# Kernel optimization log

Hardware: AMD Instinct MI355X
Metric: run time of the kernel (lower is better)

## Reference

```python
import jax, jax.numpy as jnp
import numpy as np

CUTOFF = 6.0   # matches init cutoff
D = 32         # descriptor/MLP width
NTYPES = 3     # len(type_map)


def setup_inputs() -> dict:
    key = jax.random.key(0)
    ks = jax.random.split(key, 13)
    b, n, m, n_ghost = 2, 8192, 64, 512
    neighbor_vectors = jax.random.normal(ks[0], (b, n, m, 4), jnp.float32)
    element_map = jax.random.randint(ks[1], (b, n), 0, NTYPES, jnp.int32)
    central_atoms = jax.random.randint(ks[2], (b, n), 0, n, jnp.int32)
    neighbor_indices = jax.random.randint(ks[3], (b, n, m), 0, n + n_ghost, jnp.int32)
    neighbor_types = jax.random.randint(ks[4], (b, n, m), 0, NTYPES, jnp.int32)
    type_embed = 0.1 * jax.random.normal(ks[5], (NTYPES, D), jnp.float32)
    elem_bias = 0.1 * jax.random.normal(ks[6], (NTYPES,), jnp.float32)
    W1 = 0.5 * jax.random.normal(ks[7], (4, D), jnp.float32)
    b1 = 0.1 * jax.random.normal(ks[8], (D,), jnp.float32)
    W2 = (1.0 / np.sqrt(D)) * jax.random.normal(ks[9], (D, D), jnp.float32)
    b2 = 0.1 * jax.random.normal(ks[10], (D,), jnp.float32)
    W3 = (1.0 / np.sqrt(D)) * jax.random.normal(ks[11], (D, 1), jnp.float32)
    b3 = 0.1 * jax.random.normal(ks[12], (1,), jnp.float32)
    return dict(element_map=element_map, central_atoms=central_atoms,
                neighbor_indices=neighbor_indices, neighbor_types=neighbor_types,
                neighbor_vectors=neighbor_vectors, n_ghost=n_ghost,
                type_embed=type_embed, elem_bias=elem_bias,
                W1=W1, b1=b1, W2=W2, b2=b2, W3=W3, b3=b3)


def _field_Ei(rel, element_map, neighbor_types, type_embed, elem_bias, W1, b1, W2, b2, W3, b3):
    # rel: [b,n,m,3] relative positions; recompute distance as the torch forward does
    dist = jnp.linalg.norm(rel, axis=-1, keepdims=True)                 # [b,n,m,1]
    fc = 0.5 * (jnp.cos(jnp.pi * jnp.minimum(dist, CUTOFF) / CUTOFF) + 1.0)
    s = jnp.exp(-dist) * fc                                             # smooth radial weight
    feat = jnp.concatenate([s, s * rel], axis=-1)                       # [b,n,m,4]
    h = jnp.tanh(feat @ W1 + b1 + type_embed[neighbor_types])           # [b,n,m,D]
    g = h.mean(axis=2)                                                  # pool over neighbors -> [b,n,D]
    h2 = jnp.tanh(g @ W2 + b2)                                          # [b,n,D]
    Ei = h2 @ W3 + b3 + elem_bias[element_map][..., None]               # [b,n,1]
    return Ei


def derive_mechanics(grad_Ei, neighbor_vectors, neighbor_indices, n_ghost):
    # grad_Ei: [b,n,m,3] = d(sum Ei)/d r_ij, with r_ij = r_j - r_i
    b, n, m, _ = grad_Ei.shape
    ntot = n + n_ghost
    bidx = jnp.arange(b)[:, None, None]
    # force on central atom i: +sum_j dE/dr_ij ; reaction scattered to neighbor j: -dE/dr_ij
    force = jnp.zeros((b, ntot, 3), grad_Ei.dtype)
    force = force.at[:, :n].add(grad_Ei.sum(axis=2))
    force = force.at[bidx, neighbor_indices].add(-grad_Ei)
    rij = neighbor_vectors[..., 1:]                                     # [b,n,m,3]
    pv = (rij[..., :, None] * grad_Ei[..., None, :]).reshape(b, n, m, 9)  # pair virial r (x) dE
    virial = pv.sum(axis=(1, 2))                                        # [b,9]
    av = jnp.zeros((b, ntot, 9), grad_Ei.dtype)
    av = av.at[bidx, neighbor_indices].add(pv)
    return force[:, :n], virial, av[:, :n]


def reference(element_map, central_atoms, neighbor_indices, neighbor_types,
              neighbor_vectors, n_ghost, type_embed, elem_bias,
              W1, b1, W2, b2, W3, b3):
    rel = neighbor_vectors[..., 1:]                                     # [b,n,m,3]

    def ei_sum(r):
        Ei = _field_Ei(r, element_map, neighbor_types, type_embed, elem_bias,
                       W1, b1, W2, b2, W3, b3)
        return Ei.sum(), Ei

    grad_Ei, Ei = jax.grad(ei_sum, has_aux=True)(rel)                   # matches autograd.grad w/ ones mask
    Etot = Ei.sum(axis=1)                                               # [b,1]
    dist = jnp.linalg.norm(rel, axis=-1, keepdims=True)
    nv = jnp.concatenate([dist, rel], axis=-1)
    force, virial, atomic_virial = derive_mechanics(grad_Ei, nv, neighbor_indices, n_ghost)
    return Etot, Ei, force, virial, atomic_virial
```

## Files before the change

### kernel.cpp

```cpp
#include <hip/hip_runtime.h>

#define CUTOFF_F 6.0f
#define PI_F 3.14159265358979323846f
#define CAP 112
#define EXCAP 8192

typedef __fp16 fp16x2 __attribute__((ext_vector_type(2)));

__device__ __forceinline__ unsigned pk2(float a, float b) {
  union { fp16x2 h; unsigned u; } cv;
  cv.h = __builtin_amdgcn_cvt_pkrtz(a, b);
  return cv.u;
}
__device__ __forceinline__ float f16bits(unsigned v) {
  union { unsigned short u; __fp16 h; } cv; cv.u = (unsigned short)v; return (float)cv.h;
}

template<int CTRL>
__device__ __forceinline__ float dpp_add(float x) {
  int y = __builtin_amdgcn_update_dpp(0, __float_as_int(x), CTRL, 0xf, 0xf, true);
  return x + __int_as_float(y);
}
__device__ __forceinline__ float wave_sum63(float x) {
  x = dpp_add<0x111>(x);
  x = dpp_add<0x112>(x);
  x = dpp_add<0x114>(x);
  x = dpp_add<0x118>(x);
  x = dpp_add<0x142>(x);
  x = dpp_add<0x143>(x);
  return x;
}

__device__ __forceinline__ float fast_tanh(float x) {
  float e = __expf(2.0f * x);
  return 1.0f - 2.0f * __builtin_amdgcn_rcpf(e + 1.0f);
}

__global__ __launch_bounds__(256) void field_zero(
    int* __restrict__ counts, int* __restrict__ ecount, int bn) {
  const int i = blockIdx.x * 256 + threadIdx.x;
  if (i < bn) counts[i] = 0;
  if (i == 0) ecount[0] = 0;
}

__global__ __launch_bounds__(256) void field_main(
    const int* __restrict__ element_map,
    const int* __restrict__ neighbor_indices,
    const int* __restrict__ neighbor_types,
    const float4* __restrict__ neighbor_vectors,
    const float* __restrict__ type_embed,
    const float* __restrict__ elem_bias,
    const float* __restrict__ W1,
    const float* __restrict__ b1,
    const float* __restrict__ W2,
    const float* __restrict__ b2,
    const float* __restrict__ W3,
    const float* __restrict__ b3,
    float* __restrict__ outEi,
    int* __restrict__ counts,
    int* __restrict__ ecount,
    float4* __restrict__ extras,
    float4* __restrict__ bucket,
    float* __restrict__ partials,
    int n)
{
  __shared__ float4 sW1t[32];
  __shared__ float  sbte[3][32];
  __shared__ float  sW2[32 * 33];
  __shared__ float  sW3[32];
  __shared__ float  sb2[32];
  __shared__ float  sElemBias[3];
  __shared__ float  sb3;
  __shared__ float  blkEi[4];
  __shared__ float  blkVir[4][9];
  __shared__ unsigned hb[4][64][9];
  __shared__ float    gtd[4][3][32];

  const int tid = threadIdx.x;

  if (tid < 32) {
    sW1t[tid] = make_float4(W1[tid], W1[32 + tid], W1[64 + tid], W1[96 + tid]);
    sW3[tid]  = W3[tid];
    sb2[tid]  = b2[tid];
  } else if (tid < 128) {
    int t = (tid - 32) >> 5, k = tid & 31;
    sbte[t][k] = b1[k] + type_embed[t * 32 + k];
  } else if (tid == 128) {
    sb3 = b3[0];
  } else if (tid < 132) {
    sElemBias[tid - 129] = elem_bias[tid - 129];
  }
  for (int i = tid; i < 1024; i += 256) {
    int l = i >> 5, k = i & 31;
    sW2[l * 33 + k] = W2[i];
  }
  __syncthreads();

  const int wave = tid >> 6;
  const int lane = tid & 63;
  const int atom = blockIdx.x * 4 + wave;
  const int bb = atom / n;

  const int base = atom * 64 + lane;
  const int idx = neighbor_indices[base];
  const int dest = bb * n + idx;
  const int em = element_map[atom];

  int pos = 0;
  const bool real = (idx < n);
  if (real) pos = atomicAdd(&counts[dest], 1);

  const float4 nv = neighbor_vectors[base];
  const float rx = nv.y, ry = nv.z, rz = nv.w;
  const int typ = neighbor_types[base];

  const float d2 = rx * rx + ry * ry + rz * rz;
  const float d = sqrtf(d2);
  const float invd = (d > 0.0f) ? __builtin_amdgcn_rcpf(d) : 0.0f;
  float s, sp;
  if (d < CUTOFF_F) {
    const float arg = d * (PI_F / CUTOFF_F);
    const float cs = __cosf(arg);
    const float sn = __sinf(arg);
    const float e = __expf(-d);
    const float fc = 0.5f * (cs + 1.0f);
    const float fcp = -(0.5f * PI_F / CUTOFF_F) * sn;
    s = e * fc;
    sp = e * (fcp - fc);
  } else {
    s = 0.0f;
    sp = 0.0f;
  }
  const float f1 = s * rx, f2 = s * ry, f3 = s * rz;

  float h[32];
  const int dim = lane & 15;
  const int q   = lane >> 4;
  const int w   = dim >> 1;
  const int sh  = (dim & 1) << 4;

#pragma unroll
  for (int pass = 0; pass < 2; ++pass) {
    const int kb = pass << 4;
#pragma unroll
    for (int k = 0; k < 16; k += 2) {
      const float4 wa = sW1t[kb + k];
      float pa = sbte[typ][kb + k];
      pa = fmaf(s, wa.x, pa); pa = fmaf(f1, wa.y, pa);
      pa = fmaf(f2, wa.z, pa); pa = fmaf(f3, wa.w, pa);
      h[kb + k] = fast_tanh(pa);
      const float4 wb = sW1t[kb + k + 1];
      float pb = sbte[typ][kb + k + 1];
      pb = fmaf(s, wb.x, pb); pb = fmaf(f1, wb.y, pb);
      pb = fmaf(f2, wb.z, pb); pb = fmaf(f3, wb.w, pb);
      h[kb + k + 1] = fast_tanh(pb);
      hb[wave][lane][k >> 1] = pk2(h[kb + k], h[kb + k + 1]);
    }
    float s0 = 0.0f, s1 = 0.0f;
#pragma unroll
    for (int jj = 0; jj < 16; jj += 2) {
      s0 += f16bits(hb[wave][(q << 4) + jj][w] >> sh);
      s1 += f16bits(hb[wave][(q << 4) + jj + 1][w] >> sh);
    }
    float gs = s0 + s1;
    gs += __shfl_xor(gs, 16);
    gs += __shfl_xor(gs, 32);
    if (lane < 16) gtd[wave][0][kb + lane] = gs * (1.0f / 64.0f);
  }

  const int kd = lane & 31;
  float a0 = sb2[kd], a1 = 0.0f, a2 = 0.0f, a3 = 0.0f;
#pragma unroll
  for (int l = 0; l < 8; l += 4) {
    const float4 gA = *(const float4*)&gtd[wave][0][l];
    const float4 gB = *(const float4*)&gtd[wave][0][l + 8];
    const float4 gC = *(const float4*)&gtd[wave][0][l + 16];
    const float4 gD = *(const float4*)&gtd[wave][0][l + 24];
    a0 = fmaf(gA.x, sW2[(l + 0) * 33 + kd], a0);
    a0 = fmaf(gA.y, sW2[(l + 1) * 33 + kd], a0);
    a0 = fmaf(gA.z, sW2[(l + 2) * 33 + kd], a0);
    a0 = fmaf(gA.w, sW2[(l + 3) * 33 + kd], a0);
    a1 = fmaf(gB.x, sW2[(l + 8) * 33 + kd], a1);
    a1 = fmaf(gB.y, sW2[(l + 9) * 33 + kd], a1);
    a1 = fmaf(gB.z, sW2[(l + 10) * 33 + kd], a1);
    a1 = fmaf(gB.w, sW2[(l + 11) * 33 + kd], a1);
    a2 = fmaf(gC.x, sW2[(l + 16) * 33 + kd], a2);
    a2 = fmaf(gC.y, sW2[(l + 17) * 33 + kd], a2);
    a2 = fmaf(gC.z, sW2[(l + 18) * 33 + kd], a2);
    a2 = fmaf(gC.w, sW2[(l + 19) * 33 + kd], a2);
    a3 = fmaf(gD.x, sW2[(l + 24) * 33 + kd], a3);
    a3 = fmaf(gD.y, sW2[(l + 25) * 33 + kd], a3);
    a3 = fmaf(gD.z, sW2[(l + 26) * 33 + kd], a3);
    a3 = fmaf(gD.w, sW2[(l + 27) * 33 + kd], a3);
  }
  const float acc = (a0 + a1) + (a2 + a3);
  const float h2 = fast_tanh(acc);
  const float tl = (1.0f - h2 * h2) * sW3[kd];
  if (lane < 32) gtd[wave][1][kd] = tl;

  float b0 = 0.0f, b1v = 0.0f, b2v = 0.0f, b3v = 0.0f;
#pragma unroll
  for (int l = 0; l < 8; l += 4) {
    const float4 tA = *(const float4*)&gtd[wave][1][l];
    const float4 tB = *(const float4*)&gtd[wave][1][l + 8];
    const float4 tC = *(const float4*)&gtd[wave][1][l + 16];
    const float4 tD = *(const float4*)&gtd[wave][1][l + 24];
    b0 = fmaf(tA.x, sW2[kd * 33 + l + 0], b0);
    b0 = fmaf(tA.y, sW2[kd * 33 + l + 1], b0);
    b0 = fmaf(tA.z, sW2[kd * 33 + l + 2], b0);
    b0 = fmaf(tA.w, sW2[kd * 33 + l + 3], b0);
    b1v = fmaf(tB.x, sW2[kd * 33 + l + 8], b1v);
    b1v = fmaf(tB.y, sW2[kd * 33 + l + 9], b1v);
    b1v = fmaf(tB.z, sW2[kd * 33 + l + 10], b1v);
    b1v = fmaf(tB.w, sW2[kd * 33 + l + 11], b1v);
    b2v = fmaf(tC.x, sW2[kd * 33 + l + 16], b2v);
    b2v = fmaf(tC.y, sW2[kd * 33 + l + 17], b2v);
    b2v = fmaf(tC.z, sW2[kd * 33 + l + 18], b2v);
    b2v = fmaf(tC.w, sW2[kd * 33 + l + 19], b2v);
    b3v = fmaf(tD.x, sW2[kd * 33 + l + 24], b3v);
    b3v = fmaf(tD.y, sW2[kd * 33 + l + 25], b3v);
    b3v = fmaf(tD.z, sW2[kd * 33 + l + 26], b3v);
    b3v = fmaf(tD.w, sW2[kd * 33 + l + 27], b3v);
  }
  if (lane < 32) gtd[wave][2][kd] = ((b0 + b1v) + (b2v + b3v)) * (1.0f / 64.0f);

  float p = h2 * sW3[kd];

  float q0 = 0.0f, q1 = 0.0f, q2 = 0.0f, q3 = 0.0f;
#pragma unroll
  for (int k = 0; k < 32; k += 4) {
    const float4 d4 = *(const float4*)&gtd[wave][2][k];
#pragma unroll
    for (int u = 0; u < 4; ++u) {
      const float dgk = (u == 0) ? d4.x : (u == 1) ? d4.y : (u == 2) ? d4.z : d4.w;
      const float hk = h[k + u];
      const float dpre = dgk * (1.0f - hk * hk);
      const float4 wv = sW1t[k + u];
      q0 = fmaf(dpre, wv.x, q0);
      q1 = fmaf(dpre, wv.y, q1);
      q2 = fmaf(dpre, wv.z, q2);
      q3 = fmaf(dpre, wv.w, q3);
    }
  }

  const float common = sp * invd * (q0 + q1 * rx + q2 * ry + q3 * rz);
  const float gx = fmaf(common, rx, s * q1);
  const float gy = fmaf(common, ry, s * q2);
  const float gz = fmaf(common, rz, s * q3);

  if (real) {
    float4 pay;
    pay.x = __uint_as_float(pk2(gx, gy));
    pay.y = __uint_as_float(pk2(gz, rx));
    pay.z = __uint_as_float(pk2(ry, rz));
    if (pos < CAP) {
      pay.w = 0.0f;
      bucket[(size_t)dest * CAP + pos] = pay;
    } else {
      const int ep = atomicAdd(ecount, 1);
      if (ep < EXCAP) {
        pay.w = __int_as_float(dest);
        extras[ep] = pay;
      }
    }
  }

  float sfx = wave_sum63(gx);
  float sfy = wave_sum63(gy);
  float sfz = wave_sum63(gz);
  float vr0 = wave_sum63(rx * gx), vr1 = wave_sum63(rx * gy), vr2 = wave_sum63(rx * gz);
  float vr3 = wave_sum63(ry * gx), vr4 = wave_sum63(ry * gy), vr5 = wave_sum63(ry * gz);
  float vr6 = wave_sum63(rz * gx), vr7 = wave_sum63(rz * gy), vr8 = wave_sum63(rz * gz);
  float psum = wave_sum63(p) * 0.5f;

  if (lane == 63) {
    const float Ei_val = psum + sb3 + sElemBias[em];
    outEi[atom] = Ei_val;
    blkEi[wave] = Ei_val;
    blkVir[wave][0] = vr0; blkVir[wave][1] = vr1; blkVir[wave][2] = vr2;
    blkVir[wave][3] = vr3; blkVir[wave][4] = vr4; blkVir[wave][5] = vr5;
    blkVir[wave][6] = vr6; blkVir[wave][7] = vr7; blkVir[wave][8] = vr8;
    float4 pay;
    pay.x = __uint_as_float(pk2(-sfx, -sfy));
    pay.y = __uint_as_float(pk2(-sfz, 0.0f));
    pay.z = 0.0f;
    const int spos = atomicAdd(&counts[atom], 1);
    if (spos < CAP) {
      pay.w = 0.0f;
      bucket[(size_t)atom * CAP + spos] = pay;
    } else {
      const int ep = atomicAdd(ecount, 1);
      if (ep < EXCAP) {
        pay.w = __int_as_float(atom);
        extras[ep] = pay;
      }
    }
  }

  __syncthreads();
  if (tid < 9) {
    partials[blockIdx.x * 10 + tid] =
        blkVir[0][tid] + blkVir[1][tid] + blkVir[2][tid] + blkVir[3][tid];
  } else if (tid == 9) {
    partials[blockIdx.x * 10 + 9] = blkEi[0] + blkEi[1] + blkEi[2] + blkEi[3];
  }
}

__global__ __launch_bounds__(256) void field_gather(
    const int* __restrict__ counts,
    const int* __restrict__ ecount,
    const float4* __restrict__ extras,
    const float4* __restrict__ bucket,
    const float* __restrict__ partials,
    float* __restrict__ outForce,
    float* __restrict__ outAV,
    float* __restrict__ outEtot,
    float* __restrict__ outVirial,
    int half)
{
  __shared__ float sf[4][12];
  __shared__ float sacc[4][10];
  const int tid = threadIdx.x;
  const int wave = tid >> 6;
  const int lane = tid & 63;
  const int dest = blockIdx.x * 4 + wave;

  const int rawcnt = counts[dest];
  const int cnt = (rawcnt > CAP) ? CAP : rawcnt;
  const int ec0 = *ecount;

  float fx = 0.0f, fy = 0.0f, fz = 0.0f;
  float a0 = 0, a1 = 0, a2 = 0, a3 = 0, a4 = 0, a5 = 0, a6 = 0, a7 = 0, a8 = 0;

#pragma unroll 2
  for (int l = lane; l < cnt; l += 64) {
    const float4 pay = bucket[(size_t)dest * CAP + l];
    const unsigned w0 = __float_as_uint(pay.x);
    const unsigned w1 = __float_as_uint(pay.y);
    const unsigned w2 = __float_as_uint(pay.z);
    const float gx = f16bits(w0), gy = f16bits(w0 >> 16);
    const float gz = f16bits(w1), rx = f16bits(w1 >> 16);
    const float ry = f16bits(w2), rz = f16bits(w2 >> 16);
    fx -= gx; fy -= gy; fz -= gz;
    a0 = fmaf(rx, gx, a0); a1 = fmaf(rx, gy, a1); a2 = fmaf(rx, gz, a2);
    a3 = fmaf(ry, gx, a3); a4 = fmaf(ry, gy, a4); a5 = fmaf(ry, gz, a5);
    a6 = fmaf(rz, gx, a6); a7 = fmaf(rz, gy, a7); a8 = fmaf(rz, gz, a8);
  }

  if (ec0 > 0) {
    const int ec = (ec0 < EXCAP) ? ec0 : EXCAP;
    for (int t = lane; t < ec; t += 64) {
      const float4 ex = extras[t];
      if (__float_as_int(ex.w) == dest) {
        const unsigned w0 = __float_as_uint(ex.x);
        const unsigned w1 = __float_as_uint(ex.y);
        const unsigned w2 = __float_as_uint(ex.z);
        const float gx = f16bits(w0), gy = f16bits(w0 >> 16);
        const float gz = f16bits(w1), rx = f16bits(w1 >> 16);
        const float ry = f16bits(w2), rz = f16bits(w2 >> 16);
        fx -= gx; fy -= gy; fz -= gz;
        a0 = fmaf(rx, gx, a0); a1 = fmaf(rx, gy, a1); a2 = fmaf(rx, gz, a2);
        a3 = fmaf(ry, gx, a3); a4 = fmaf(ry, gy, a4); a5 = fmaf(ry, gz, a5);
        a6 = fmaf(rz, gx, a6); a7 = fmaf(rz, gy, a7); a8 = fmaf(rz, gz, a8);
      }
    }
  }

  fx = wave_sum63(fx); fy = wave_sum63(fy); fz = wave_sum63(fz);
  a0 = wave_sum63(a0); a1 = wave_sum63(a1); a2 = wave_sum63(a2);
  a3 = wave_sum63(a3); a4 = wave_sum63(a4); a5 = wave_sum63(a5);
  a6 = wave_sum63(a6); a7 = wave_sum63(a7); a8 = wave_sum63(a8);

  if (lane == 63) {
    sf[wave][0] = fx; sf[wave][1] = fy; sf[wave][2] = fz;
    sf[wave][3] = a0; sf[wave][4] = a1; sf[wave][5] = a2;
    sf[wave][6] = a3; sf[wave][7] = a4; sf[wave][8] = a5;
    sf[wave][9] = a6; sf[wave][10] = a7; sf[wave][11] = a8;
  }
  __syncthreads();

  const int d0 = blockIdx.x * 4;
  if (tid < 12) {
    outForce[(size_t)d0 * 3 + tid] = sf[tid / 3][tid % 3];
  } else if (tid >= 64 && tid < 100) {
    const int t = tid - 64;
    outAV[(size_t)d0 * 9 + t] = sf[t / 9][3 + t % 9];
  }

  if (blockIdx.x < 2) {
    const int b = blockIdx.x;
    float acc[10] = {0, 0, 0, 0, 0, 0, 0, 0, 0, 0};
    for (int r = b * half + tid; r < (b + 1) * half; r += 256) {
#pragma unroll
      for (int t = 0; t < 10; ++t) acc[t] += partials[r * 10 + t];
    }
#pragma unroll
    for (int t = 0; t < 10; ++t) acc[t] = wave_sum63(acc[t]);
    if (lane == 63) {
#pragma unroll
      for (int t = 0; t < 10; ++t) sacc[wave][t] = acc[t];
    }
    __syncthreads();
    if (tid < 9) {
      outVirial[b * 9 + tid] = sacc[0][tid] + sacc[1][tid] + sacc[2][tid] + sacc[3][tid];
    } else if (tid == 9) {
      outEtot[b] = sacc[0][9] + sacc[1][9] + sacc[2][9] + sacc[3][9];
    }
  }
}

extern "C" void kernel_launch(void* const* d_in, const int* in_sizes, int n_in,
                              void* d_out, int out_size, void* d_ws, size_t ws_size,
                              hipStream_t stream) {
  const int* element_map        = (const int*)d_in[0];
  const int* neighbor_indices   = (const int*)d_in[2];
  const int* neighbor_types     = (const int*)d_in[3];
  const float4* neighbor_vectors = (const float4*)d_in[4];
  const float* type_embed = (const float*)d_in[6];
  const float* elem_bias  = (const float*)d_in[7];
  const float* W1 = (const float*)d_in[8];
  const float* b1 = (const float*)d_in[9];
  const float* W2 = (const float*)d_in[10];
  const float* b2 = (const float*)d_in[11];
  const float* W3 = (const float*)d_in[12];
  const float* b3 = (const float*)d_in[13];

  const int B = 2;
  const int bn = in_sizes[0];
  const int n = bn / B;
  const int nblk = bn / 4;

  float* out = (float*)d_out;
  float* outEtot   = out;
  float* outEi     = outEtot + B;
  float* outForce  = outEi + bn;
  float* outVirial = outForce + (size_t)bn * 3;
  float* outAV     = outVirial + (size_t)B * 9;

  char* ws = (char*)d_ws;
  int* counts = (int*)ws;
  size_t countBytes = (size_t)bn * sizeof(int);
  int* ecount = (int*)(ws + countBytes);
  size_t ecountBytes = 16;
  float4* extras = (float4*)(ws + countBytes + ecountBytes);
  size_t extrasBytes = (size_t)EXCAP * sizeof(float4);
  float* partials = (float*)(ws + countBytes + ecountBytes + extrasBytes);
  size_t partialBytes = (size_t)nblk * 10 * sizeof(float);
  float4* bucket = (float4*)(ws + countBytes + ecountBytes + extrasBytes + partialBytes);

  dim3 block(256);
  hipLaunchKernelGGL(field_zero, dim3((bn + 255) / 256), block, 0, stream,
                     counts, ecount, bn);
  hipLaunchKernelGGL(field_main, dim3(nblk), block, 0, stream,
                     element_map, neighbor_indices, neighbor_types,
                     neighbor_vectors, type_embed, elem_bias,
                     W1, b1, W2, b2, W3, b3,
                     outEi, counts, ecount, extras, bucket, partials, n);
  hipLaunchKernelGGL(field_gather, dim3(nblk), block, 0, stream,
                     counts, ecount, extras, bucket, partials,
                     outForce, outAV, outEtot, outVirial, nblk / B);
}
```

Before: 147.6 us.

## Use packed fp16 dot2 and half2 math for per-neighbor MLP forward/backward

After: 148.9 us. No clear change (+0.8%).

```diff
diff --git a/kernel.cpp b/kernel.cpp
--- a/kernel.cpp
+++ b/kernel.cpp
@@ -5,15 +5,28 @@
 #define CAP 112
 #define EXCAP 8192
 
-typedef __fp16 fp16x2 __attribute__((ext_vector_type(2)));
+typedef __fp16   fp16x2 __attribute__((ext_vector_type(2)));
+typedef _Float16 h2f    __attribute__((ext_vector_type(2)));
+
+union hcv { unsigned u; fp16x2 b; h2f a; };
+__device__ __forceinline__ unsigned as_u(h2f x)   { hcv c; c.a = x; return c.u; }
+__device__ __forceinline__ h2f      u2a(unsigned v){ hcv c; c.u = v; return c.a; }
+__device__ __forceinline__ fp16x2   u2b(unsigned v){ hcv c; c.u = v; return c.b; }
 
 __device__ __forceinline__ unsigned pk2(float a, float b) {
-  union { fp16x2 h; unsigned u; } cv;
-  cv.h = __builtin_amdgcn_cvt_pkrtz(a, b);
-  return cv.u;
+  hcv c; c.b = __builtin_amdgcn_cvt_pkrtz(a, b); return c.u;
 }
 __device__ __forceinline__ float f16bits(unsigned v) {
   union { unsigned short u; __fp16 h; } cv; cv.u = (unsigned short)v; return (float)cv.h;
+}
+
+__device__ __forceinline__ float FDOT2(unsigned a, unsigned b, float c) {
+#if defined(__has_builtin) && __has_builtin(__builtin_amdgcn_fdot2)
+  return __builtin_amdgcn_fdot2(u2b(a), u2b(b), c, false);
+#else
+  h2f x = u2a(a), y = u2a(b);
+  return fmaf((float)x.x, (float)y.x, fmaf((float)x.y, (float)y.y, c));
+#endif
 }
 
 template<int CTRL>
@@ -64,35 +77,51 @@
     float* __restrict__ partials,
     int n)
 {
-  __shared__ float4 sW1t[32];
-  __shared__ float  sbte[3][32];
-  __shared__ float  sW2[32 * 33];
+  __shared__ uint4  sW1f[16];
+  __shared__ uint4  sW1b[16];
+  __shared__ unsigned sW2h[16*33];
+  __shared__ unsigned sW2d[32*17];
+  __shared__ float2 sbte2[3][16];
   __shared__ float  sW3[32];
   __shared__ float  sb2[32];
   __shared__ float  sElemBias[3];
   __shared__ float  sb3;
   __shared__ float  blkEi[4];
   __shared__ float  blkVir[4][9];
-  __shared__ unsigned hb[4][64][9];
-  __shared__ float    gtd[4][3][32];
+  __shared__ unsigned hb[4][64][5];
+  __shared__ unsigned sgp[4][16];
+  __shared__ unsigned stl[4][16];
+  __shared__ unsigned sdg[4][16];
 
   const int tid = threadIdx.x;
 
-  if (tid < 32) {
-    sW1t[tid] = make_float4(W1[tid], W1[32 + tid], W1[64 + tid], W1[96 + tid]);
-    sW3[tid]  = W3[tid];
-    sb2[tid]  = b2[tid];
-  } else if (tid < 128) {
-    int t = (tid - 32) >> 5, k = tid & 31;
-    sbte[t][k] = b1[k] + type_embed[t * 32 + k];
-  } else if (tid == 128) {
+  if (tid < 32) { sW3[tid] = W3[tid]; sb2[tid] = b2[tid]; }
+  if (tid < 16) {
+    const int k0 = 2*tid, k1 = 2*tid + 1;
+    sW1f[tid] = make_uint4(pk2(W1[k0],    W1[32+k0]),
+                           pk2(W1[64+k0], W1[96+k0]),
+                           pk2(W1[k1],    W1[32+k1]),
+                           pk2(W1[64+k1], W1[96+k1]));
+  } else if (tid < 32) {
+    const int p = tid - 16, k0 = 2*p, k1 = 2*p + 1;
+    sW1b[p] = make_uint4(pk2(W1[k0],    W1[k1]),
+                         pk2(W1[32+k0], W1[32+k1]),
+                         pk2(W1[64+k0], W1[64+k1]),
+                         pk2(W1[96+k0], W1[96+k1]));
+  } else if (tid < 80) {
+    const int i = tid - 32, t = i >> 4, pp = i & 15;
+    sbte2[t][pp] = make_float2(b1[2*pp]   + type_embed[t*32 + 2*pp],
+                               b1[2*pp+1] + type_embed[t*32 + 2*pp+1]);
+  } else if (tid == 80) {
     sb3 = b3[0];
-  } else if (tid < 132) {
-    sElemBias[tid - 129] = elem_bias[tid - 129];
-  }
-  for (int i = tid; i < 1024; i += 256) {
-    int l = i >> 5, k = i & 31;
-    sW2[l * 33 + k] = W2[i];
+  } else if (tid < 84) {
+    sElemBias[tid - 81] = elem_bias[tid - 81];
+  }
+  for (int i = tid; i < 512; i += 256) {
+    const int p = i >> 5, kd = i & 31;
+    sW2h[p*33 + kd] = pk2(W2[(2*p)*32 + kd], W2[(2*p+1)*32 + kd]);
+    const int l = i >> 4, pp = i & 15;
+    sW2d[l*17 + pp] = pk2(W2[l*32 + 2*pp], W2[l*32 + 2*pp + 1]);
   }
   __syncthreads();
 
@@ -132,115 +161,87 @@
     sp = 0.0f;
   }
   const float f1 = s * rx, f2 = s * ry, f3 = s * rz;
-
-  float h[32];
-  const int dim = lane & 15;
-  const int q   = lane >> 4;
-  const int w   = dim >> 1;
-  const int sh  = (dim & 1) << 4;
-
-#pragma unroll
-  for (int pass = 0; pass < 2; ++pass) {
-    const int kb = pass << 4;
-#pragma unroll
-    for (int k = 0; k < 16; k += 2) {
-      const float4 wa = sW1t[kb + k];
-      float pa = sbte[typ][kb + k];
-      pa = fmaf(s, wa.x, pa); pa = fmaf(f1, wa.y, pa);
-      pa = fmaf(f2, wa.z, pa); pa = fmaf(f3, wa.w, pa);
-      h[kb + k] = fast_tanh(pa);
-      const float4 wb = sW1t[kb + k + 1];
-      float pb = sbte[typ][kb + k + 1];
-      pb = fmaf(s, wb.x, pb); pb = fmaf(f1, wb.y, pb);
-      pb = fmaf(f2, wb.z, pb); pb = fmaf(f3, wb.w, pb);
-      h[kb + k + 1] = fast_tanh(pb);
-      hb[wave][lane][k >> 1] = pk2(h[kb + k], h[kb + k + 1]);
-    }
-    float s0 = 0.0f, s1 = 0.0f;
-#pragma unroll
-    for (int jj = 0; jj < 16; jj += 2) {
-      s0 += f16bits(hb[wave][(q << 4) + jj][w] >> sh);
-      s1 += f16bits(hb[wave][(q << 4) + jj + 1][w] >> sh);
-    }
-    float gs = s0 + s1;
-    gs += __shfl_xor(gs, 16);
-    gs += __shfl_xor(gs, 32);
-    if (lane < 16) gtd[wave][0][kb + lane] = gs * (1.0f / 64.0f);
+  const unsigned sf01 = pk2(s, f1);
+  const unsigned f23  = pk2(f2, f3);
+
+  unsigned hpz[16];
+  const int pair2 = lane & 3;
+  const int grp   = lane >> 2;
+
+#pragma unroll
+  for (int P = 0; P < 4; ++P) {
+#pragma unroll
+    for (int e = 0; e < 4; ++e) {
+      const int p = 4*P + e;
+      const uint4 wq = sW1f[p];
+      const float2 bt = sbte2[typ][p];
+      float pre0 = FDOT2(sf01, wq.x, bt.x);
+      pre0 = FDOT2(f23, wq.y, pre0);
+      float pre1 = FDOT2(sf01, wq.z, bt.y);
+      pre1 = FDOT2(f23, wq.w, pre1);
+      const unsigned hp = pk2(fast_tanh(pre0), fast_tanh(pre1));
+      hpz[p] = hp;
+      hb[wave][lane][e] = hp;
+    }
+    h2f acc = u2a(hb[wave][grp*4 + 0][pair2]);
+    acc = acc + u2a(hb[wave][grp*4 + 1][pair2]);
+    acc = acc + u2a(hb[wave][grp*4 + 2][pair2]);
+    acc = acc + u2a(hb[wave][grp*4 + 3][pair2]);
+    acc = acc + u2a((unsigned)__shfl_xor((int)as_u(acc), 4));
+    acc = acc + u2a((unsigned)__shfl_xor((int)as_u(acc), 8));
+    acc = acc + u2a((unsigned)__shfl_xor((int)as_u(acc), 16));
+    acc = acc + u2a((unsigned)__shfl_xor((int)as_u(acc), 32));
+    if (lane < 4) {
+      const h2f g2 = acc * (_Float16)(1.0f / 64.0f);
+      sgp[wave][4*P + lane] = as_u(g2);
+    }
   }
 
   const int kd = lane & 31;
-  float a0 = sb2[kd], a1 = 0.0f, a2 = 0.0f, a3 = 0.0f;
-#pragma unroll
-  for (int l = 0; l < 8; l += 4) {
-    const float4 gA = *(const float4*)&gtd[wave][0][l];
-    const float4 gB = *(const float4*)&gtd[wave][0][l + 8];
-    const float4 gC = *(const float4*)&gtd[wave][0][l + 16];
-    const float4 gD = *(const float4*)&gtd[wave][0][l + 24];
-    a0 = fmaf(gA.x, sW2[(l + 0) * 33 + kd], a0);
-    a0 = fmaf(gA.y, sW2[(l + 1) * 33 + kd], a0);
-    a0 = fmaf(gA.z, sW2[(l + 2) * 33 + kd], a0);
-    a0 = fmaf(gA.w, sW2[(l + 3) * 33 + kd], a0);
-    a1 = fmaf(gB.x, sW2[(l + 8) * 33 + kd], a1);
-    a1 = fmaf(gB.y, sW2[(l + 9) * 33 + kd], a1);
-    a1 = fmaf(gB.z, sW2[(l + 10) * 33 + kd], a1);
-    a1 = fmaf(gB.w, sW2[(l + 11) * 33 + kd], a1);
-    a2 = fmaf(gC.x, sW2[(l + 16) * 33 + kd], a2);
-    a2 = fmaf(gC.y, sW2[(l + 17) * 33 + kd], a2);
-    a2 = fmaf(gC.z, sW2[(l + 18) * 33 + kd], a2);
-    a2 = fmaf(gC.w, sW2[(l + 19) * 33 + kd], a2);
-    a3 = fmaf(gD.x, sW2[(l + 24) * 33 + kd], a3);
-    a3 = fmaf(gD.y, sW2[(l + 25) * 33 + kd], a3);
-    a3 = fmaf(gD.z, sW2[(l + 26) * 33 + kd], a3);
-    a3 = fmaf(gD.w, sW2[(l + 27) * 33 + kd], a3);
-  }
-  const float acc = (a0 + a1) + (a2 + a3);
-  const float h2 = fast_tanh(acc);
-  const float tl = (1.0f - h2 * h2) * sW3[kd];
-  if (lane < 32) gtd[wave][1][kd] = tl;
-
-  float b0 = 0.0f, b1v = 0.0f, b2v = 0.0f, b3v = 0.0f;
-#pragma unroll
-  for (int l = 0; l < 8; l += 4) {
-    const float4 tA = *(const float4*)&gtd[wave][1][l];
-    const float4 tB = *(const float4*)&gtd[wave][1][l + 8];
-    const float4 tC = *(const float4*)&gtd[wave][1][l + 16];
-    const float4 tD = *(const float4*)&gtd[wave][1][l + 24];
-    b0 = fmaf(tA.x, sW2[kd * 33 + l + 0], b0);
-    b0 = fmaf(tA.y, sW2[kd * 33 + l + 1], b0);
-    b0 = fmaf(tA.z, sW2[kd * 33 + l + 2], b0);
-    b0 = fmaf(tA.w, sW2[kd * 33 + l + 3], b0);
-    b1v = fmaf(tB.x, sW2[kd * 33 + l + 8], b1v);
-    b1v = fmaf(tB.y, sW2[kd * 33 + l + 9], b1v);
-    b1v = fmaf(tB.z, sW2[kd * 33 + l + 10], b1v);
-    b1v = fmaf(tB.w, sW2[kd * 33 + l + 11], b1v);
-    b2v = fmaf(tC.x, sW2[kd * 33 + l + 16], b2v);
-    b2v = fmaf(tC.y, sW2[kd * 33 + l + 17], b2v);
-    b2v = fmaf(tC.z, sW2[kd * 33 + l + 18], b2v);
-    b2v = fmaf(tC.w, sW2[kd * 33 + l + 19], b2v);
-    b3v = fmaf(tD.x, sW2[kd * 33 + l + 24], b3v);
-    b3v = fmaf(tD.y, sW2[kd * 33 + l + 25], b3v);
-    b3v = fmaf(tD.z, sW2[kd * 33 + l + 26], b3v);
-    b3v = fmaf(tD.w, sW2[kd * 33 + l + 27], b3v);
-  }
-  if (lane < 32) gtd[wave][2][kd] = ((b0 + b1v) + (b2v + b3v)) * (1.0f / 64.0f);
-
-  float p = h2 * sW3[kd];
-
+  const int hh = lane >> 5;
+  float acc0 = 0.0f, acc1 = 0.0f;
+#pragma unroll
+  for (int j = 0; j < 8; j += 2) {
+    const int p = hh*8 + j;
+    acc0 = FDOT2(sgp[wave][p],     sW2h[p*33 + kd],       acc0);
+    acc1 = FDOT2(sgp[wave][p + 1], sW2h[(p + 1)*33 + kd], acc1);
+  }
+  float accs = acc0 + acc1;
+  accs += __shfl_xor(accs, 32);
+  accs += sb2[kd];
+  const float h2v = fast_tanh(accs);
+  const float tl = (1.0f - h2v * h2v) * sW3[kd];
+  const float tlo = __shfl_xor(tl, 1);
+  if (lane < 32 && !(kd & 1)) stl[wave][kd >> 1] = pk2(tl, tlo);
+
+  float d0 = 0.0f, d1 = 0.0f;
+#pragma unroll
+  for (int j = 0; j < 8; j += 2) {
+    const int p = hh*8 + j;
+    d0 = FDOT2(stl[wave][p],     sW2d[kd*17 + p],     d0);
+    d1 = FDOT2(stl[wave][p + 1], sW2d[kd*17 + p + 1], d1);
+  }
+  float dgs = (d0 + d1);
+  dgs += __shfl_xor(dgs, 32);
+  dgs *= (1.0f / 64.0f);
+  const float dgo = __shfl_xor(dgs, 1);
+  if (lane < 32 && !(kd & 1)) sdg[wave][kd >> 1] = pk2(dgs, dgo);
+
+  const float pEi = h2v * sW3[kd];
+
+  const h2f one16 = {(_Float16)1.0f, (_Float16)1.0f};
   float q0 = 0.0f, q1 = 0.0f, q2 = 0.0f, q3 = 0.0f;
 #pragma unroll
-  for (int k = 0; k < 32; k += 4) {
-    const float4 d4 = *(const float4*)&gtd[wave][2][k];
-#pragma unroll
-    for (int u = 0; u < 4; ++u) {
-      const float dgk = (u == 0) ? d4.x : (u == 1) ? d4.y : (u == 2) ? d4.z : d4.w;
-      const float hk = h[k + u];
-      const float dpre = dgk * (1.0f - hk * hk);
-      const float4 wv = sW1t[k + u];
-      q0 = fmaf(dpre, wv.x, q0);
-      q1 = fmaf(dpre, wv.y, q1);
-      q2 = fmaf(dpre, wv.z, q2);
-      q3 = fmaf(dpre, wv.w, q3);
-    }
+  for (int p = 0; p < 16; ++p) {
+    const h2f hp = u2a(hpz[p]);
+    const h2f omh = one16 - hp * hp;
+    const h2f dpre = u2a(sdg[wave][p]) * omh;
+    const uint4 wq = sW1b[p];
+    const unsigned du = as_u(dpre);
+    q0 = FDOT2(du, wq.x, q0);
+    q1 = FDOT2(du, wq.y, q1);
+    q2 = FDOT2(du, wq.z, q2);
+    q3 = FDOT2(du, wq.w, q3);
   }
 
   const float common = sp * invd * (q0 + q1 * rx + q2 * ry + q3 * rz);
@@ -258,10 +259,7 @@
       bucket[(size_t)dest * CAP + pos] = pay;
     } else {
       const int ep = atomicAdd(ecount, 1);
-      if (ep < EXCAP) {
-        pay.w = __int_as_float(dest);
-        extras[ep] = pay;
-      }
+      if (ep < EXCAP) { pay.w = __int_as_float(dest); extras[ep] = pay; }
     }
   }
 
@@ -271,7 +269,7 @@
   float vr0 = wave_sum63(rx * gx), vr1 = wave_sum63(rx * gy), vr2 = wave_sum63(rx * gz);
   float vr3 = wave_sum63(ry * gx), vr4 = wave_sum63(ry * gy), vr5 = wave_sum63(ry * gz);
   float vr6 = wave_sum63(rz * gx), vr7 = wave_sum63(rz * gy), vr8 = wave_sum63(rz * gz);
-  float psum = wave_sum63(p) * 0.5f;
+  float psum = wave_sum63(pEi) * 0.5f;
 
   if (lane == 63) {
     const float Ei_val = psum + sb3 + sElemBias[em];
@@ -290,10 +288,7 @@
       bucket[(size_t)atom * CAP + spos] = pay;
     } else {
       const int ep = atomicAdd(ecount, 1);
-      if (ep < EXCAP) {
-        pay.w = __int_as_float(atom);
-        extras[ep] = pay;
-      }
+      if (ep < EXCAP) { pay.w = __int_as_float(atom); extras[ep] = pay; }
     }
   }
 
```
